# Kernel tuning notes

Measured on AMD Instinct MI355X. Metric: run time of the kernel, lower is better.

The kernel has to match this reference:

```python
import jax, jax.numpy as jnp
import numpy as np

N_CAT, IN, H, OUT = 1024, 1024, 2048, 32000


def _lstm_cell(x, h, c, w_ih, w_hh, b_ih, b_hh):
    # x: [1, D], h/c: [1, H]; PyTorch gate order: i, f, g, o
    gates = x @ w_ih.T + b_ih + h @ w_hh.T + b_hh  # [1, 4H]
    i, f, g, o = jnp.split(gates, 4, axis=-1)
    i = jax.nn.sigmoid(i)
    f = jax.nn.sigmoid(f)
    g = jnp.tanh(g)
    o = jax.nn.sigmoid(o)
    c_new = f * c + i * g
    h_new = o * jnp.tanh(c_new)
    return h_new, c_new


def setup_inputs() -> dict:
    key = jax.random.key(0)
    ks = jax.random.split(key, 16)
    s = 0.02
    return {
        "category": jax.random.normal(ks[0], (1, N_CAT), jnp.float32),
        "input": jax.random.normal(ks[1], (1, IN), jnp.float32),
        "hidden": jax.random.normal(ks[2], (2, 1, H), jnp.float32),
        "cell_state": jax.random.normal(ks[3], (2, 1, H), jnp.float32),
        # LSTM layer 0: input dim = N_CAT + IN
        "w_ih_l0": jax.random.normal(ks[4], (4 * H, N_CAT + IN), jnp.float32) * s,
        "w_hh_l0": jax.random.normal(ks[5], (4 * H, H), jnp.float32) * s,
        "b_ih_l0": jax.random.normal(ks[6], (4 * H,), jnp.float32) * s,
        "b_hh_l0": jax.random.normal(ks[7], (4 * H,), jnp.float32) * s,
        # LSTM layer 1: input dim = H
        "w_ih_l1": jax.random.normal(ks[8], (4 * H, H), jnp.float32) * s,
        "w_hh_l1": jax.random.normal(ks[9], (4 * H, H), jnp.float32) * s,
        "b_ih_l1": jax.random.normal(ks[10], (4 * H,), jnp.float32) * s,
        "b_hh_l1": jax.random.normal(ks[11], (4 * H,), jnp.float32) * s,
        # output linear: [OUT, N_CAT + H]
        "w_out": jax.random.normal(ks[12], (OUT, N_CAT + H), jnp.float32) * s,
        "b_out": jax.random.normal(ks[13], (OUT,), jnp.float32) * s,
    }


def reference(category, input, hidden, cell_state,
              w_ih_l0, w_hh_l0, b_ih_l0, b_hh_l0,
              w_ih_l1, w_hh_l1, b_ih_l1, b_hh_l1,
              w_out, b_out):
    # single-step, batch=1, seq=1; dropout layers are identity (eval mode)
    x = jnp.concatenate([category, input], axis=-1)  # [1, N_CAT+IN]
    h1, c1 = _lstm_cell(x, hidden[0], cell_state[0], w_ih_l0, w_hh_l0, b_ih_l0, b_hh_l0)
    h2, c2 = _lstm_cell(h1, hidden[1], cell_state[1], w_ih_l1, w_hh_l1, b_ih_l1, b_hh_l1)
    out_comb = jnp.concatenate([category, h2], axis=-1)  # [1, N_CAT+H]
    logits = out_comb @ w_out.T + b_out  # [1, OUT]
    logp = jax.nn.log_softmax(logits, axis=1)
    new_hidden = jnp.stack([h1, h2], axis=0)      # [2, 1, H]
    new_cell = jnp.stack([c1, c2], axis=0)        # [2, 1, H]
    return logp, new_hidden, new_cell
```

## Files before the change

kernel.cpp:

```cpp
#include <hip/hip_runtime.h>
#include <math.h>

#define HDIM 2048
#define OUTN 32000
#define KOUT 3072
#define NPART 2000

__device__ __forceinline__ float wave_reduce_sum(float v) {
    #pragma unroll
    for (int off = 32; off > 0; off >>= 1)
        v += __shfl_down(v, off, 64);
    return v;
}

__device__ __forceinline__ float dot4(float4 a, float4 b) {
    return a.x * b.x + a.y * b.y + a.z * b.z + a.w * b.w;
}

typedef float nfloat4 __attribute__((ext_vector_type(4)));
__device__ __forceinline__ float4 ldnt4(const float4* p) {
    nfloat4 v = __builtin_nontemporal_load((const nfloat4*)p);
    return make_float4(v.x, v.y, v.z, v.w);
}

__device__ __forceinline__ float sigmoidf_(float x) {
    return 1.0f / (1.0f + __expf(-x));
}

__global__ __launch_bounds__(256) void lstm_gemv(
    const float* __restrict__ xa,
    const float* __restrict__ xb,
    const float* __restrict__ h,
    const float* __restrict__ w_ih,
    const float* __restrict__ w_hh,
    const float* __restrict__ b_ih,
    const float* __restrict__ b_hh,
    float* __restrict__ gates)
{
    const int wave = threadIdx.x >> 6;
    const int lane = threadIdx.x & 63;
    const int g    = blockIdx.x * 4 + wave;
    const int r0   = g * 4;

    const float4* wi  = (const float4*)(w_ih + (size_t)r0 * HDIM);
    const float4* wh  = (const float4*)(w_hh + (size_t)r0 * HDIM);
    const float4* xa4 = (const float4*)xa;
    const float4* xb4 = (const float4*)xb;
    const float4* h4  = (const float4*)h;

    float a0 = 0.f, a1 = 0.f, a2 = 0.f, a3 = 0.f;
    #pragma unroll
    for (int it = 0; it < 8; ++it) {
        const int k4 = it * 64 + lane;
        float4 xv = (it < 4) ? xa4[k4] : xb4[k4 - 256];
        a0 += dot4(ldnt4(&wi[k4]),        xv);
        a1 += dot4(ldnt4(&wi[k4 + 512]),  xv);
        a2 += dot4(ldnt4(&wi[k4 + 1024]), xv);
        a3 += dot4(ldnt4(&wi[k4 + 1536]), xv);
    }
    #pragma unroll
    for (int it = 0; it < 8; ++it) {
        const int k4 = it * 64 + lane;
        float4 hv = h4[k4];
        a0 += dot4(ldnt4(&wh[k4]),        hv);
        a1 += dot4(ldnt4(&wh[k4 + 512]),  hv);
        a2 += dot4(ldnt4(&wh[k4 + 1024]), hv);
        a3 += dot4(ldnt4(&wh[k4 + 1536]), hv);
    }
    a0 = wave_reduce_sum(a0);
    a1 = wave_reduce_sum(a1);
    a2 = wave_reduce_sum(a2);
    a3 = wave_reduce_sum(a3);

    if (lane == 0) {
        float4 bi = ((const float4*)b_ih)[g];
        float4 bh = ((const float4*)b_hh)[g];
        ((float4*)gates)[g] = make_float4(a0 + bi.x + bh.x,
                                          a1 + bi.y + bh.y,
                                          a2 + bi.z + bh.z,
                                          a3 + bi.w + bh.w);
    }
}

__global__ __launch_bounds__(256) void lstm_point(
    const float* __restrict__ gates,
    const float* __restrict__ c,
    float* __restrict__ h_out,
    float* __restrict__ c_out)
{
    const int n = blockIdx.x * 256 + threadIdx.x;
    float gi = sigmoidf_(gates[n]);
    float gf = sigmoidf_(gates[HDIM + n]);
    float gg = tanhf(gates[2 * HDIM + n]);
    float go = sigmoidf_(gates[3 * HDIM + n]);
    float cn = gf * c[n] + gi * gg;
    float hn = go * tanhf(cn);
    c_out[n] = cn;
    h_out[n] = hn;
}

__global__ __launch_bounds__(256) void logits_kernel(
    const float* __restrict__ cat,
    const float* __restrict__ h2,
    const float* __restrict__ w_out,
    const float* __restrict__ b_out,
    float* __restrict__ logits,
    float2* __restrict__ partial)
{
    const int wave = threadIdx.x >> 6;
    const int lane = threadIdx.x & 63;
    const int row0 = blockIdx.x * 16 + wave * 4;

    const float4* w4 = (const float4*)(w_out + (size_t)row0 * KOUT);
    const float4* c4 = (const float4*)cat;
    const float4* h4 = (const float4*)h2;

    float a0 = 0.f, a1 = 0.f, a2 = 0.f, a3 = 0.f;
    #pragma unroll
    for (int it = 0; it < 12; ++it) {
        const int k4 = it * 64 + lane;
        float4 v = (it < 4) ? c4[k4] : h4[k4 - 256];
        a0 += dot4(ldnt4(&w4[k4]),        v);
        a1 += dot4(ldnt4(&w4[k4 + 768]),  v);
        a2 += dot4(ldnt4(&w4[k4 + 1536]), v);
        a3 += dot4(ldnt4(&w4[k4 + 2304]), v);
    }
    a0 = wave_reduce_sum(a0);
    a1 = wave_reduce_sum(a1);
    a2 = wave_reduce_sum(a2);
    a3 = wave_reduce_sum(a3);

    __shared__ float sm[4], ss[4];
    if (lane == 0) {
        a0 += b_out[row0];
        a1 += b_out[row0 + 1];
        a2 += b_out[row0 + 2];
        a3 += b_out[row0 + 3];
        *(float4*)(logits + row0) = make_float4(a0, a1, a2, a3);
        float m = fmaxf(fmaxf(a0, a1), fmaxf(a2, a3));
        float s = __expf(a0 - m) + __expf(a1 - m) + __expf(a2 - m) + __expf(a3 - m);
        sm[wave] = m; ss[wave] = s;
    }
    __syncthreads();
    if (threadIdx.x == 0) {
        float M = sm[0], S = ss[0];
        #pragma unroll
        for (int w = 1; w < 4; ++w) {
            float mn = fmaxf(M, sm[w]);
            S = S * __expf(M - mn) + ss[w] * __expf(sm[w] - mn);
            M = mn;
        }
        partial[blockIdx.x] = make_float2(M, S);
    }
}

__global__ __launch_bounds__(1024) void lse_combine(
    const float2* __restrict__ partial, float* __restrict__ logz)
{
    float m = -INFINITY, s = 0.f;
    for (int i = threadIdx.x; i < NPART; i += 1024) {
        float2 p  = partial[i];
        float  mn = fmaxf(m, p.x);
        s = s * __expf(m - mn) + p.y * __expf(p.x - mn);
        m = mn;
    }
    #pragma unroll
    for (int off = 32; off > 0; off >>= 1) {
        float m2 = __shfl_down(m, off, 64);
        float s2 = __shfl_down(s, off, 64);
        float mn = fmaxf(m, m2);
        s = s * __expf(m - mn) + s2 * __expf(m2 - mn);
        m = mn;
    }
    __shared__ float smm[16], sss[16];
    const int wave = threadIdx.x >> 6;
    const int lane = threadIdx.x & 63;
    if (lane == 0) { smm[wave] = m; sss[wave] = s; }
    __syncthreads();
    if (threadIdx.x == 0) {
        float M = smm[0], S = sss[0];
        for (int w = 1; w < 16; ++w) {
            float mn = fmaxf(M, smm[w]);
            S = S * __expf(M - mn) + sss[w] * __expf(smm[w] - mn);
            M = mn;
        }
        *logz = M + logf(S);
    }
}

__global__ __launch_bounds__(256) void sub_kernel(
    const float* __restrict__ logits, const float* __restrict__ logz,
    float* __restrict__ out)
{
    const int i = blockIdx.x * 256 + threadIdx.x;
    out[i] = logits[i] - *logz;
}

extern "C" void kernel_launch(void* const* d_in, const int* in_sizes, int n_in,
                              void* d_out, int out_size, void* d_ws, size_t ws_size,
                              hipStream_t stream) {
    const float* category = (const float*)d_in[0];
    const float* input    = (const float*)d_in[1];
    const float* hidden   = (const float*)d_in[2];
    const float* cell     = (const float*)d_in[3];
    const float* w_ih_l0  = (const float*)d_in[4];
    const float* w_hh_l0  = (const float*)d_in[5];
    const float* b_ih_l0  = (const float*)d_in[6];
    const float* b_hh_l0  = (const float*)d_in[7];
    const float* w_ih_l1  = (const float*)d_in[8];
    const float* w_hh_l1  = (const float*)d_in[9];
    const float* b_ih_l1  = (const float*)d_in[10];
    const float* b_hh_l1  = (const float*)d_in[11];
    const float* w_out    = (const float*)d_in[12];
    const float* b_out    = (const float*)d_in[13];

    float* out  = (float*)d_out;
    float* logp = out;
    float* h1   = out + OUTN;
    float* h2   = out + OUTN + HDIM;
    float* c1   = out + OUTN + 2 * HDIM;
    float* c2   = out + OUTN + 3 * HDIM;

    float* gates  = (float*)d_ws;
    float* logits = gates + 4 * HDIM;
    float* logz   = logits + OUTN;
    float2* partial = (float2*)logp;

    lstm_gemv<<<512, 256, 0, stream>>>(category, input, hidden,
                                       w_ih_l0, w_hh_l0, b_ih_l0, b_hh_l0,
                                       gates);
    lstm_point<<<8, 256, 0, stream>>>(gates, cell, h1, c1);
    lstm_gemv<<<512, 256, 0, stream>>>(h1, h1 + 1024, hidden + HDIM,
                                       w_ih_l1, w_hh_l1, b_ih_l1, b_hh_l1,
                                       gates);
    lstm_point<<<8, 256, 0, stream>>>(gates, cell + HDIM, h2, c2);

    logits_kernel<<<NPART, 256, 0, stream>>>(category, h2, w_out, b_out,
                                             logits, partial);
    lse_combine<<<1, 1024, 0, stream>>>(partial, logz);
    sub_kernel<<<OUTN / 256, 256, 0, stream>>>(logits, logz, logp);
}
```

Measured before the change: 652.3 us.

## Fuse LSE combine into subtraction kernel and widen logits rows per wave

Each wave in the logits GEMV now computes 8 output rows instead of 4, halving the block count and the number of partial max/sum pairs. The single-block LSE combine kernel is removed. Every block of the final subtraction kernel now recomputes the log-sum-exp from the 1000 partials and subtracts it. This drops one serialized single-block launch, at the cost of redundant reduction work in each of 125 blocks and more registers and loads in flight per wave. Partials move from the output buffer to workspace.

```diff
diff --git a/kernel.cpp b/kernel.cpp
--- a/kernel.cpp
+++ b/kernel.cpp
@@ -4,7 +4,7 @@
 #define HDIM 2048
 #define OUTN 32000
 #define KOUT 3072
-#define NPART 2000
+#define NPART 1000
 
 __device__ __forceinline__ float wave_reduce_sum(float v) {
     #pragma unroll
@@ -109,36 +109,38 @@
 {
     const int wave = threadIdx.x >> 6;
     const int lane = threadIdx.x & 63;
-    const int row0 = blockIdx.x * 16 + wave * 4;
+    const int row0 = blockIdx.x * 32 + wave * 8;
 
     const float4* w4 = (const float4*)(w_out + (size_t)row0 * KOUT);
     const float4* c4 = (const float4*)cat;
     const float4* h4 = (const float4*)h2;
 
-    float a0 = 0.f, a1 = 0.f, a2 = 0.f, a3 = 0.f;
+    float a[8] = {0.f, 0.f, 0.f, 0.f, 0.f, 0.f, 0.f, 0.f};
     #pragma unroll
     for (int it = 0; it < 12; ++it) {
         const int k4 = it * 64 + lane;
         float4 v = (it < 4) ? c4[k4] : h4[k4 - 256];
-        a0 += dot4(ldnt4(&w4[k4]),        v);
-        a1 += dot4(ldnt4(&w4[k4 + 768]),  v);
-        a2 += dot4(ldnt4(&w4[k4 + 1536]), v);
-        a3 += dot4(ldnt4(&w4[k4 + 2304]), v);
-    }
-    a0 = wave_reduce_sum(a0);
-    a1 = wave_reduce_sum(a1);
-    a2 = wave_reduce_sum(a2);
-    a3 = wave_reduce_sum(a3);
+        #pragma unroll
+        for (int r = 0; r < 8; ++r)
+            a[r] += dot4(ldnt4(&w4[k4 + r * 768]), v);
+    }
+    #pragma unroll
+    for (int r = 0; r < 8; ++r)
+        a[r] = wave_reduce_sum(a[r]);
 
     __shared__ float sm[4], ss[4];
     if (lane == 0) {
-        a0 += b_out[row0];
-        a1 += b_out[row0 + 1];
-        a2 += b_out[row0 + 2];
-        a3 += b_out[row0 + 3];
-        *(float4*)(logits + row0) = make_float4(a0, a1, a2, a3);
-        float m = fmaxf(fmaxf(a0, a1), fmaxf(a2, a3));
-        float s = __expf(a0 - m) + __expf(a1 - m) + __expf(a2 - m) + __expf(a3 - m);
+        #pragma unroll
+        for (int r = 0; r < 8; ++r)
+            a[r] += b_out[row0 + r];
+        *(float4*)(logits + row0)     = make_float4(a[0], a[1], a[2], a[3]);
+        *(float4*)(logits + row0 + 4) = make_float4(a[4], a[5], a[6], a[7]);
+        float m = a[0];
+        #pragma unroll
+        for (int r = 1; r < 8; ++r) m = fmaxf(m, a[r]);
+        float s = 0.f;
+        #pragma unroll
+        for (int r = 0; r < 8; ++r) s += __expf(a[r] - m);
         sm[wave] = m; ss[wave] = s;
     }
     __syncthreads();
@@ -154,11 +156,13 @@
     }
 }
 
-__global__ __launch_bounds__(1024) void lse_combine(
-    const float2* __restrict__ partial, float* __restrict__ logz)
+__global__ __launch_bounds__(256) void sub_fused(
+    const float* __restrict__ logits,
+    const float2* __restrict__ partial,
+    float* __restrict__ out)
 {
     float m = -INFINITY, s = 0.f;
-    for (int i = threadIdx.x; i < NPART; i += 1024) {
+    for (int i = threadIdx.x; i < NPART; i += 256) {
         float2 p  = partial[i];
         float  mn = fmaxf(m, p.x);
         s = s * __expf(m - mn) + p.y * __expf(p.x - mn);
@@ -172,28 +176,24 @@
         s = s * __expf(m - mn) + s2 * __expf(m2 - mn);
         m = mn;
     }
-    __shared__ float smm[16], sss[16];
+    __shared__ float smm[4], sss[4], s_logz;
     const int wave = threadIdx.x >> 6;
     const int lane = threadIdx.x & 63;
     if (lane == 0) { smm[wave] = m; sss[wave] = s; }
     __syncthreads();
     if (threadIdx.x == 0) {
         float M = smm[0], S = sss[0];
-        for (int w = 1; w < 16; ++w) {
+        #pragma unroll
+        for (int w = 1; w < 4; ++w) {
             float mn = fmaxf(M, smm[w]);
             S = S * __expf(M - mn) + sss[w] * __expf(smm[w] - mn);
             M = mn;
         }
-        *logz = M + logf(S);
-    }
-}
-
-__global__ __launch_bounds__(256) void sub_kernel(
-    const float* __restrict__ logits, const float* __restrict__ logz,
-    float* __restrict__ out)
-{
+        s_logz = M + logf(S);
+    }
+    __syncthreads();
     const int i = blockIdx.x * 256 + threadIdx.x;
-    out[i] = logits[i] - *logz;
+    out[i] = logits[i] - s_logz;
 }
 
 extern "C" void kernel_launch(void* const* d_in, const int* in_sizes, int n_in,
@@ -221,10 +221,9 @@
     float* c1   = out + OUTN + 2 * HDIM;
     float* c2   = out + OUTN + 3 * HDIM;
 
-    float* gates  = (float*)d_ws;
-    float* logits = gates + 4 * HDIM;
-    float* logz   = logits + OUTN;
-    float2* partial = (float2*)logp;
+    float* gates    = (float*)d_ws;
+    float* logits   = gates + 4 * HDIM;
+    float2* partial = (float2*)(logits + OUTN);
 
     lstm_gemv<<<512, 256, 0, stream>>>(category, input, hidden,
                                        w_ih_l0, w_hh_l0, b_ih_l0, b_hh_l0,
@@ -237,6 +236,5 @@
 
     logits_kernel<<<NPART, 256, 0, stream>>>(category, h2, w_out, b_out,
                                              logits, partial);
-    lse_combine<<<1, 1024, 0, stream>>>(partial, logz);
-    sub_kernel<<<OUTN / 256, 256, 0, stream>>>(logits, logz, logp);
-}
+    sub_fused<<<OUTN / 256, 256, 0, stream>>>(logits, partial, logp);
+}
```

After: 652.1 us. No clear change (-0.0%).
